# Optimization experiments

Measured on AMD Instinct MI355X. Metric: run time of the kernel, lower is better.

The kernel has to match this reference:

```python
import jax, jax.numpy as jnp
import numpy as np

N_EMBD = 1024
N_HEAD = 16
HEAD_DIM = N_EMBD // N_HEAD


def setup_inputs() -> dict:
    key = jax.random.key(0)
    ks = jax.random.split(key, 5)
    B, T, C = 2, 2048, N_EMBD
    scale = 0.02
    return {
        "x": jax.random.normal(ks[0], (B, T, C), dtype=jnp.float32),
        "w_attn": jax.random.normal(ks[1], (C, 3 * C), dtype=jnp.float32) * scale,
        "b_attn": jax.random.normal(ks[2], (3 * C,), dtype=jnp.float32) * scale,
        "w_proj": jax.random.normal(ks[3], (C, C), dtype=jnp.float32) * scale,
        "b_proj": jax.random.normal(ks[4], (C,), dtype=jnp.float32) * scale,
    }


def reference(x, w_attn, b_attn, w_proj, b_proj):
    B, T, C = x.shape
    H, D = N_HEAD, HEAD_DIM
    qkv = x @ w_attn + b_attn  # [B,T,3C]
    q, k, v = jnp.split(qkv, 3, axis=-1)
    # [B,T,C] -> [B,H,T,D]
    q = q.reshape(B, T, H, D).transpose(0, 2, 1, 3)
    k = k.reshape(B, T, H, D).transpose(0, 2, 1, 3)
    v = v.reshape(B, T, H, D).transpose(0, 2, 1, 3)
    scores = jnp.einsum("bhqd,bhkd->bhqk", q, k) / jnp.sqrt(jnp.float32(D))
    causal = jnp.tril(jnp.ones((T, T), dtype=bool))
    scores = jnp.where(causal, scores, jnp.finfo(scores.dtype).min)
    attn = jax.nn.softmax(scores, axis=-1)
    y = jnp.einsum("bhqk,bhkd->bhqd", attn, v)  # [B,H,T,D]
    y = y.transpose(0, 2, 1, 3).reshape(B, T, C)
    return y @ w_proj + b_proj
```

## Files before the change

kernel.cpp:

```cpp
#include <hip/hip_runtime.h>

typedef unsigned short u16;
typedef u16 u16x4 __attribute__((ext_vector_type(4)));
typedef u16 u16x8 __attribute__((ext_vector_type(8)));
typedef __bf16 bf16x8 __attribute__((ext_vector_type(8)));
typedef float floatx4 __attribute__((ext_vector_type(4)));

#define N_EMBD 1024
#define N_HEAD 16
#define HEAD_DIM 64
#define SEQ 2048
#define BATCH 2
#define M_ROWS (BATCH * SEQ)

typedef __attribute__((address_space(1))) const unsigned char ga_t;
typedef __attribute__((address_space(3))) unsigned char la_t;

#if __has_builtin(__builtin_amdgcn_exp2f)
#define EXP2(x) __builtin_amdgcn_exp2f(x)
#else
#define EXP2(x) exp2f(x)
#endif

__device__ __forceinline__ u16 cvt_bf16(float f) {
  return __builtin_bit_cast(u16, (__bf16)f);
}

__global__ __launch_bounds__(256) void prep(const float* __restrict__ x,
                                            u16* __restrict__ xb,
                                            const float* __restrict__ wa,
                                            const float* __restrict__ wp,
                                            u16* __restrict__ outa,
                                            u16* __restrict__ outp) {
  const int bid = blockIdx.x;
  if (bid < 2048) {
    const long i = ((long)bid * 256 + threadIdx.x) * 8;
    const float4 f0 = *(const float4*)&x[i];
    const float4 f1 = *(const float4*)&x[i + 4];
    u16x8 p;
    p[0] = cvt_bf16(f0.x); p[1] = cvt_bf16(f0.y);
    p[2] = cvt_bf16(f0.z); p[3] = cvt_bf16(f0.w);
    p[4] = cvt_bf16(f1.x); p[5] = cvt_bf16(f1.y);
    p[6] = cvt_bf16(f1.z); p[7] = cvt_bf16(f1.w);
    *(u16x8*)&xb[i] = p;
    return;
  }
  __shared__ u16 tile[32][33];
  const int t = bid - 2048;
  const int gx = t & 127;
  const int gy = t >> 7;
  const int R = N_EMBD;
  const float* in;
  u16* out;
  int C, bx;
  if (gx < 96) {
    in = wa; out = outa; C = 3 * N_EMBD; bx = gx * 32;
  } else {
    in = wp; out = outp; C = N_EMBD; bx = (gx - 96) * 32;
  }
  const int by = gy * 32;
  const int tx = threadIdx.x & 31;
  const int ty = threadIdx.x >> 5;
#pragma unroll
  for (int j = 0; j < 32; j += 8)
    tile[ty + j][tx] = cvt_bf16(in[(long)(by + ty + j) * C + bx + tx]);
  __syncthreads();
#pragma unroll
  for (int j = 0; j < 32; j += 8)
    out[(long)(bx + ty + j) * R + by + tx] = tile[tx][ty + j];
}

#define BK 32

template <int MODE>
__global__ __launch_bounds__(256) void gemm128(
    const u16* __restrict__ A, const u16* __restrict__ Bt,
    const float* __restrict__ bias, float* __restrict__ out,
    u16* __restrict__ qo, u16* __restrict__ ko, u16* __restrict__ vo, int N,
    int K) {
  __shared__ u16 As[128 * BK];
  __shared__ u16 Bs[128 * BK];
  const int tid = threadIdx.x;
  const int bm = blockIdx.y * 128;
  const int bn = blockIdx.x * 128;
  const int w = tid >> 6;
  const int l = tid & 63;
  const int wm = (w >> 1) * 64;
  const int wn = (w & 1) * 64;
  const int m16 = l & 15;
  const int quad = l >> 4;
  const int lrow = l >> 2;
  const int lcol = (l & 3) * 8;

  floatx4 acc[4][4];
#pragma unroll
  for (int i = 0; i < 4; ++i)
#pragma unroll
    for (int j = 0; j < 4; ++j) acc[i][j] = (floatx4){0.f, 0.f, 0.f, 0.f};

  for (int kt = 0; kt < K; kt += BK) {
#pragma unroll
    for (int p = 0; p < 2; ++p) {
      const int arow = p * 64 + w * 16;
      long gA;
      if (MODE == 0) {
        gA = (long)(bm + arow + lrow) * K + kt + lcol;
      } else {
        const int m = bm + arow + lrow;
        const int b = m >> 11, t = m & 2047;
        const int k0 = kt + lcol;
        const int head = k0 >> 6, dd = k0 & 63;
        gA = (((long)(b * N_HEAD + head)) * SEQ + t) * HEAD_DIM + dd;
      }
      __builtin_amdgcn_global_load_lds((ga_t*)(A + gA), (la_t*)&As[arow * BK],
                                       16, 0, 0);
      const long gB = (long)(bn + arow + lrow) * K + kt + lcol;
      __builtin_amdgcn_global_load_lds((ga_t*)(Bt + gB), (la_t*)&Bs[arow * BK],
                                       16, 0, 0);
    }
    __syncthreads();

    bf16x8 af[4], bfr[4];
#pragma unroll
    for (int i = 0; i < 4; ++i)
      af[i] = __builtin_bit_cast(
          bf16x8, *(const u16x8*)&As[(wm + i * 16 + m16) * BK + quad * 8]);
#pragma unroll
    for (int j = 0; j < 4; ++j)
      bfr[j] = __builtin_bit_cast(
          bf16x8, *(const u16x8*)&Bs[(wn + j * 16 + m16) * BK + quad * 8]);
#pragma unroll
    for (int i = 0; i < 4; ++i)
#pragma unroll
      for (int j = 0; j < 4; ++j)
        acc[i][j] = __builtin_amdgcn_mfma_f32_16x16x32_bf16(af[i], bfr[j],
                                                            acc[i][j], 0, 0, 0);
    __syncthreads();
  }

#pragma unroll
  for (int i = 0; i < 4; ++i) {
#pragma unroll
    for (int j = 0; j < 4; ++j) {
      const int col = bn + wn + j * 16 + m16;
      const float bv = bias[col];
      if (MODE == 1) {
#pragma unroll
        for (int r = 0; r < 4; ++r) {
          const int row = bm + wm + i * 16 + quad * 4 + r;
          out[(long)row * N_EMBD + col] = acc[i][j][r] + bv;
        }
      } else {
        const int which = col >> 10;
        const int cc = col & 1023;
        const int h = cc >> 6;
        const int dd = cc & 63;
        const int row0 = bm + wm + i * 16 + quad * 4;
        const int b = row0 >> 11;
        const int t0 = row0 & 2047;
        if (which == 2) {
          u16x4 pk;
#pragma unroll
          for (int r = 0; r < 4; ++r) pk[r] = cvt_bf16(acc[i][j][r] + bv);
          *(u16x4*)&vo[(((long)(b * N_HEAD + h)) * HEAD_DIM + dd) * SEQ + t0] =
              pk;
        } else {
          u16* dst = (which == 0) ? qo : ko;
#pragma unroll
          for (int r = 0; r < 4; ++r)
            dst[(((long)(b * N_HEAD + h)) * SEQ + t0 + r) * HEAD_DIM + dd] =
                cvt_bf16(acc[i][j][r] + bv);
        }
      }
    }
  }
}

#define BQ 64
#define BKV 64
#define KPAD 72
#define LOG2E 1.44269504f
#define NQT (SEQ / BQ)

__device__ __forceinline__ void load_kv(const u16* __restrict__ K,
                                        const u16* __restrict__ Vt, long bh,
                                        int kt, int tid, u16x8 kreg[2],
                                        u16x8 vreg[2]) {
#pragma unroll
  for (int i = 0; i < 2; ++i) {
    const int p = tid + 256 * i;
    const int kkey = p >> 3, kdg = p & 7;
    kreg[i] = *(const u16x8*)&K[(bh * SEQ + kt + kkey) * HEAD_DIM + kdg * 8];
    const int vd = p >> 3, vkg = (p & 7) * 8;
    vreg[i] = *(const u16x8*)&Vt[(bh * HEAD_DIM + vd) * SEQ + kt + vkg];
  }
}

__global__ __launch_bounds__(256) void flash_attn(u16* __restrict__ Qy,
                                                  const u16* __restrict__ K,
                                                  const u16* __restrict__ Vt) {
  const int id = blockIdx.x;
  const int iq = (NQT - 1) - (id >> 5);
  const int bh_ = ((id >> 3) & 3) * 8 + (id & 7);
  const long bh = bh_;
  const int tid = threadIdx.x;
  const int w = tid >> 6;
  const int l = tid & 63;
  const int m16 = l & 15;
  const int quad = l >> 4;

  __shared__ u16 Kl[2][BKV * KPAD];
  __shared__ u16 Vl[2][HEAD_DIM * KPAD];
  __shared__ u16 Pl[4][16 * KPAD];

  const float SC = 0.125f * LOG2E;

  const int qb = iq * BQ;
  const int ntiles = iq + 1;
  const int qglob = qb + w * 16 + m16;

  bf16x8 qf[2];
  {
    const u16* qrow = Qy + (bh * SEQ + qglob) * HEAD_DIM;
    qf[0] = __builtin_bit_cast(bf16x8, *(const u16x8*)&qrow[quad * 8]);
    qf[1] = __builtin_bit_cast(bf16x8, *(const u16x8*)&qrow[32 + quad * 8]);
  }

  floatx4 Oacc[4];
#pragma unroll
  for (int t = 0; t < 4; ++t) Oacc[t] = (floatx4){0.f, 0.f, 0.f, 0.f};
  float mrow = -1e30f, lrow = 0.f;

  u16x8 kreg[2], vreg[2];
  load_kv(K, Vt, bh, 0, tid, kreg, vreg);

  for (int it = 0; it < ntiles; ++it) {
    const int buf = it & 1;
#pragma unroll
    for (int i = 0; i < 2; ++i) {
      const int p = tid + 256 * i;
      const int kkey = p >> 3, kdg = p & 7;
      *(u16x8*)&Kl[buf][kkey * KPAD + kdg * 8] = kreg[i];
      const int vd = p >> 3, vkg = (p & 7) * 8;
      *(u16x8*)&Vl[buf][vd * KPAD + vkg] = vreg[i];
    }
    __syncthreads();
    if (it + 1 < ntiles) load_kv(K, Vt, bh, (it + 1) * BKV, tid, kreg, vreg);

    floatx4 s[4];
#pragma unroll
    for (int j = 0; j < 4; ++j) s[j] = (floatx4){0.f, 0.f, 0.f, 0.f};
#pragma unroll
    for (int j = 0; j < 4; ++j)
#pragma unroll
      for (int kk = 0; kk < 2; ++kk) {
        const bf16x8 kf = __builtin_bit_cast(
            bf16x8, *(const u16x8*)&Kl[buf][(j * 16 + m16) * KPAD + kk * 32 +
                                            quad * 8]);
        s[j] = __builtin_amdgcn_mfma_f32_16x16x32_bf16(kf, qf[kk], s[j], 0, 0,
                                                       0);
      }
    if (it == ntiles - 1) {
      const int kt = it * BKV;
#pragma unroll
      for (int j = 0; j < 4; ++j) {
        const int key0 = kt + j * 16 + quad * 4;
#pragma unroll
        for (int r = 0; r < 4; ++r)
          if (key0 + r > qglob) s[j][r] = -1e30f;
      }
    }

    float tm = s[0][0];
#pragma unroll
    for (int j = 0; j < 4; ++j)
#pragma unroll
      for (int r = 0; r < 4; ++r) tm = fmaxf(tm, s[j][r]);
    tm = fmaxf(tm, __shfl_xor(tm, 16, 64));
    tm = fmaxf(tm, __shfl_xor(tm, 32, 64));
    const float mn = fmaxf(mrow, tm * SC);
    const float al = EXP2(mrow - mn);
    mrow = mn;

    float ls = 0.f;
#pragma unroll
    for (int j = 0; j < 4; ++j) {
      u16x4 pk;
#pragma unroll
      for (int r = 0; r < 4; ++r) {
        const float p = EXP2(__builtin_fmaf(s[j][r], SC, -mn));
        ls += p;
        pk[r] = cvt_bf16(p);
      }
      *(u16x4*)&Pl[w][m16 * KPAD + j * 16 + quad * 4] = pk;
    }
    ls += __shfl_xor(ls, 16, 64);
    ls += __shfl_xor(ls, 32, 64);
    lrow = lrow * al + ls;
#pragma unroll
    for (int t = 0; t < 4; ++t)
#pragma unroll
      for (int r = 0; r < 4; ++r) Oacc[t][r] *= al;

    bf16x8 pf[2];
    pf[0] = __builtin_bit_cast(bf16x8,
                               *(const u16x8*)&Pl[w][m16 * KPAD + quad * 8]);
    pf[1] = __builtin_bit_cast(
        bf16x8, *(const u16x8*)&Pl[w][m16 * KPAD + 32 + quad * 8]);
#pragma unroll
    for (int t = 0; t < 4; ++t)
#pragma unroll
      for (int kk = 0; kk < 2; ++kk) {
        const bf16x8 vf = __builtin_bit_cast(
            bf16x8, *(const u16x8*)&Vl[buf][(t * 16 + m16) * KPAD + kk * 32 +
                                            quad * 8]);
        Oacc[t] = __builtin_amdgcn_mfma_f32_16x16x32_bf16(vf, pf[kk], Oacc[t],
                                                          0, 0, 0);
      }
  }

  const float invl = 1.f / lrow;
#pragma unroll
  for (int t = 0; t < 4; ++t) {
    u16x4 pk;
#pragma unroll
    for (int r = 0; r < 4; ++r) pk[r] = cvt_bf16(Oacc[t][r] * invl);
    *(u16x4*)&Qy[(bh * SEQ + qglob) * HEAD_DIM + t * 16 + quad * 4] = pk;
  }
}

extern "C" void kernel_launch(void* const* d_in, const int* in_sizes, int n_in,
                              void* d_out, int out_size, void* d_ws,
                              size_t ws_size, hipStream_t stream) {
  const float* x = (const float*)d_in[0];
  const float* w_attn = (const float*)d_in[1];
  const float* b_attn = (const float*)d_in[2];
  const float* w_proj = (const float*)d_in[3];
  const float* b_proj = (const float*)d_in[4];
  float* out = (float*)d_out;

  char* ws = (char*)d_ws;
  const size_t SZ = (size_t)BATCH * N_HEAD * SEQ * HEAD_DIM * sizeof(u16);
  u16* q = (u16*)(ws);
  u16* k = (u16*)(ws + SZ);
  u16* vT = (u16*)(ws + 2 * SZ);
  u16* wT_a = (u16*)(ws + 3 * SZ);
  u16* wT_p = (u16*)(ws + 3 * SZ + (size_t)3 * N_EMBD * N_EMBD * sizeof(u16));
  u16* xb = (u16*)(ws + 3 * SZ + (size_t)4 * N_EMBD * N_EMBD * sizeof(u16));

  prep<<<2048 + 4096, 256, 0, stream>>>(x, xb, w_attn, w_proj, wT_a, wT_p);

  gemm128<0><<<dim3(3 * N_EMBD / 128, M_ROWS / 128), 256, 0, stream>>>(
      xb, wT_a, b_attn, nullptr, q, k, vT, 3 * N_EMBD, N_EMBD);

  flash_attn<<<NQT * 32, 256, 0, stream>>>(q, k, vT);

  gemm128<1><<<dim3(N_EMBD / 128, M_ROWS / 128), 256, 0, stream>>>(
      q, wT_p, b_proj, out, nullptr, nullptr, nullptr, N_EMBD, N_EMBD);
}
```

Measured before the change: 187.5 us.

## Load V fragments directly from global, add lazy softmax rescale, raise occupancy hint

V tiles are no longer staged through shared memory. Each wave now reads its V MFMA operands straight from global memory into registers at the start of each tile, which removes the V LDS buffer, its stores and its reads. The online softmax now rescales the running max, sum and O accumulator only when some row's new max exceeds the old one by more than 4 in log2 space. Otherwise it skips those multiplies. Launch bounds now ask for 4 blocks per CU, and the smaller LDS footprint helps reach that. The trade-off is uncoalesced, latency-exposed global reads for V, plus a warp-uniform branch in the inner loop.

```diff
diff --git a/kernel.cpp b/kernel.cpp
--- a/kernel.cpp
+++ b/kernel.cpp
@@ -182,23 +182,9 @@
 #define LOG2E 1.44269504f
 #define NQT (SEQ / BQ)
 
-__device__ __forceinline__ void load_kv(const u16* __restrict__ K,
-                                        const u16* __restrict__ Vt, long bh,
-                                        int kt, int tid, u16x8 kreg[2],
-                                        u16x8 vreg[2]) {
-#pragma unroll
-  for (int i = 0; i < 2; ++i) {
-    const int p = tid + 256 * i;
-    const int kkey = p >> 3, kdg = p & 7;
-    kreg[i] = *(const u16x8*)&K[(bh * SEQ + kt + kkey) * HEAD_DIM + kdg * 8];
-    const int vd = p >> 3, vkg = (p & 7) * 8;
-    vreg[i] = *(const u16x8*)&Vt[(bh * HEAD_DIM + vd) * SEQ + kt + vkg];
-  }
-}
-
-__global__ __launch_bounds__(256) void flash_attn(u16* __restrict__ Qy,
-                                                  const u16* __restrict__ K,
-                                                  const u16* __restrict__ Vt) {
+__global__ __launch_bounds__(256, 4) void flash_attn(
+    u16* __restrict__ Qy, const u16* __restrict__ K,
+    const u16* __restrict__ Vt) {
   const int id = blockIdx.x;
   const int iq = (NQT - 1) - (id >> 5);
   const int bh_ = ((id >> 3) & 3) * 8 + (id & 7);
@@ -210,7 +196,6 @@
   const int quad = l >> 4;
 
   __shared__ u16 Kl[2][BKV * KPAD];
-  __shared__ u16 Vl[2][HEAD_DIM * KPAD];
   __shared__ u16 Pl[4][16 * KPAD];
 
   const float SC = 0.125f * LOG2E;
@@ -231,21 +216,43 @@
   for (int t = 0; t < 4; ++t) Oacc[t] = (floatx4){0.f, 0.f, 0.f, 0.f};
   float mrow = -1e30f, lrow = 0.f;
 
-  u16x8 kreg[2], vreg[2];
-  load_kv(K, Vt, bh, 0, tid, kreg, vreg);
+  u16x8 kreg[2];
+#pragma unroll
+  for (int i = 0; i < 2; ++i) {
+    const int p = tid + 256 * i;
+    const int kkey = p >> 3, kdg = p & 7;
+    kreg[i] = *(const u16x8*)&K[(bh * SEQ + kkey) * HEAD_DIM + kdg * 8];
+  }
 
   for (int it = 0; it < ntiles; ++it) {
     const int buf = it & 1;
+    const int kt = it * BKV;
 #pragma unroll
     for (int i = 0; i < 2; ++i) {
       const int p = tid + 256 * i;
       const int kkey = p >> 3, kdg = p & 7;
       *(u16x8*)&Kl[buf][kkey * KPAD + kdg * 8] = kreg[i];
-      const int vd = p >> 3, vkg = (p & 7) * 8;
-      *(u16x8*)&Vl[buf][vd * KPAD + vkg] = vreg[i];
     }
     __syncthreads();
-    if (it + 1 < ntiles) load_kv(K, Vt, bh, (it + 1) * BKV, tid, kreg, vreg);
+    if (it + 1 < ntiles) {
+#pragma unroll
+      for (int i = 0; i < 2; ++i) {
+        const int p = tid + 256 * i;
+        const int kkey = p >> 3, kdg = p & 7;
+        kreg[i] = *(const u16x8*)&K[(bh * SEQ + (it + 1) * BKV + kkey) *
+                                        HEAD_DIM +
+                                    kdg * 8];
+      }
+    }
+
+    bf16x8 vf[4][2];
+#pragma unroll
+    for (int t = 0; t < 4; ++t)
+#pragma unroll
+      for (int kk = 0; kk < 2; ++kk)
+        vf[t][kk] = __builtin_bit_cast(
+            bf16x8, *(const u16x8*)&Vt[(bh * HEAD_DIM + t * 16 + m16) * SEQ +
+                                       kt + kk * 32 + quad * 8]);
 
     floatx4 s[4];
 #pragma unroll
@@ -261,7 +268,6 @@
                                                        0);
       }
     if (it == ntiles - 1) {
-      const int kt = it * BKV;
 #pragma unroll
       for (int j = 0; j < 4; ++j) {
         const int key0 = kt + j * 16 + quad * 4;
@@ -278,9 +284,17 @@
       for (int r = 0; r < 4; ++r) tm = fmaxf(tm, s[j][r]);
     tm = fmaxf(tm, __shfl_xor(tm, 16, 64));
     tm = fmaxf(tm, __shfl_xor(tm, 32, 64));
-    const float mn = fmaxf(mrow, tm * SC);
-    const float al = EXP2(mrow - mn);
-    mrow = mn;
+    const float pm = tm * SC;
+    if (!__all(pm <= mrow + 4.f)) {
+      const float mn = fmaxf(mrow, pm);
+      const float al = EXP2(mrow - mn);
+      mrow = mn;
+      lrow *= al;
+#pragma unroll
+      for (int t = 0; t < 4; ++t)
+#pragma unroll
+        for (int r = 0; r < 4; ++r) Oacc[t][r] *= al;
+    }
 
     float ls = 0.f;
 #pragma unroll
@@ -288,7 +302,7 @@
       u16x4 pk;
 #pragma unroll
       for (int r = 0; r < 4; ++r) {
-        const float p = EXP2(__builtin_fmaf(s[j][r], SC, -mn));
+        const float p = EXP2(__builtin_fmaf(s[j][r], SC, -mrow));
         ls += p;
         pk[r] = cvt_bf16(p);
       }
@@ -296,11 +310,7 @@
     }
     ls += __shfl_xor(ls, 16, 64);
     ls += __shfl_xor(ls, 32, 64);
-    lrow = lrow * al + ls;
-#pragma unroll
-    for (int t = 0; t < 4; ++t)
-#pragma unroll
-      for (int r = 0; r < 4; ++r) Oacc[t][r] *= al;
+    lrow += ls;
 
     bf16x8 pf[2];
     pf[0] = __builtin_bit_cast(bf16x8,
@@ -310,13 +320,9 @@
 #pragma unroll
     for (int t = 0; t < 4; ++t)
 #pragma unroll
-      for (int kk = 0; kk < 2; ++kk) {
-        const bf16x8 vf = __builtin_bit_cast(
-            bf16x8, *(const u16x8*)&Vl[buf][(t * 16 + m16) * KPAD + kk * 32 +
-                                            quad * 8]);
-        Oacc[t] = __builtin_amdgcn_mfma_f32_16x16x32_bf16(vf, pf[kk], Oacc[t],
-                                                          0, 0, 0);
-      }
+      for (int kk = 0; kk < 2; ++kk)
+        Oacc[t] = __builtin_amdgcn_mfma_f32_16x16x32_bf16(vf[t][kk], pf[kk],
+                                                          Oacc[t], 0, 0, 0);
   }
 
   const float invl = 1.f / lrow;
```

After: 230.3 us. 1.23x slower.
